# Kernel optimization log

Hardware: AMD Instinct MI355X
Metric: run time of the kernel (lower is better)

The kernel has to match this reference:

```python
import jax, jax.numpy as jnp
import numpy as np

P, H, T, B = 16, 24, 168, 4096


def _lstm(x, W_ih, W_hh, b_ih, b_hh):
    # x: [B, T, F]; PyTorch gate order i, f, g, o; returns all hidden states [B, T, H]
    Bsz = x.shape[0]
    Hd = W_hh.shape[1]
    # batch the input GEMM over all timesteps
    xg = jnp.einsum('btf,gf->btg', x, W_ih) + b_ih + b_hh  # [B, T, 4H]

    def step(carry, xt):
        h, c = carry
        g = xt + h @ W_hh.T  # [B, 4H]
        i, f, gg, o = jnp.split(g, 4, axis=-1)
        c = jax.nn.sigmoid(f) * c + jax.nn.sigmoid(i) * jnp.tanh(gg)
        h = jax.nn.sigmoid(o) * jnp.tanh(c)
        return (h, c), h

    h0 = jnp.zeros((Bsz, Hd), x.dtype)
    _, hs = jax.lax.scan(step, (h0, h0), jnp.swapaxes(xg, 0, 1))
    return jnp.swapaxes(hs, 0, 1)  # [B, T, H]


def setup_inputs() -> dict:
    key = jax.random.key(0)
    ks = jax.random.split(key, 14)
    s1 = 1.0 / np.sqrt(H)
    u = lambda k, shape: jax.random.uniform(k, shape, jnp.float32, -s1, s1)
    return {
        'x': jax.random.normal(ks[0], (B, T, P), jnp.float32),
        'W_ih1': u(ks[1], (4 * H, P)), 'W_hh1': u(ks[2], (4 * H, H)),
        'b_ih1': u(ks[3], (4 * H,)), 'b_hh1': u(ks[4], (4 * H,)),
        'W_ih2': u(ks[5], (4 * H, H)), 'W_hh2': u(ks[6], (4 * H, H)),
        'b_ih2': u(ks[7], (4 * H,)), 'b_hh2': u(ks[8], (4 * H,)),
        'W1': u(ks[9], (16, H)), 'b1': u(ks[10], (16,)),
        'W2': u(ks[11], (H, 16)), 'b2': u(ks[12], (H,)),
    }


def reference(x, W_ih1, W_hh1, b_ih1, b_hh1, W_ih2, W_hh2, b_ih2, b_hh2, W1, b1, W2, b2):
    h = jnp.tanh(_lstm(x, W_ih1, W_hh1, b_ih1, b_hh1))       # [B, T, H]
    h = jnp.tanh(_lstm(h, W_ih2, W_hh2, b_ih2, b_hh2))       # [B, T, H]
    h = h[:, -1, :]                                           # [B, H]
    h = jax.nn.relu(h @ W1.T + b1)                            # [B, 16]; dropout = identity (eval mode)
    out = h @ W2.T + b2                                       # [B, 24]
    return out.reshape(out.shape[0], -1, 1)                   # [B, 24, 1]
```

## Files before the change

### kernel.cpp

```cpp
#include <hip/hip_runtime.h>

constexpr int T = 168;
constexpr int P = 16;
constexpr int H = 24;

typedef float v2f __attribute__((ext_vector_type(2)));

__device__ __forceinline__ v2f mk2(float a, float b) { v2f r; r[0] = a; r[1] = b; return r; }
__device__ __forceinline__ v2f bc2(float a)          { v2f r; r[0] = a; r[1] = a; return r; }
__device__ __forceinline__ v2f pkfma(v2f a, v2f b, v2f c) {
    return __builtin_elementwise_fma(a, b, c);
}

__device__ __forceinline__ float rcp_f(float x) { return __builtin_amdgcn_rcpf(x); }
__device__ __forceinline__ float sigm_f(float x) { return rcp_f(1.f + __expf(-x)); }
__device__ __forceinline__ float tanh_fast(float x) {
    return fmaf(2.f, rcp_f(1.f + __expf(-2.f * x)), -1.f);
}

#define KEEP2(v) asm volatile("" : "+v"(v))
#define LDS_SYNC() asm volatile("s_waitcnt lgkmcnt(0)" ::: "memory")

#define PK4(acc_, v4_, w_, b_) do {                       \
    acc_ = pkfma(bc2((v4_).x), (w_)[(b_)],     acc_);     \
    acc_ = pkfma(bc2((v4_).y), (w_)[(b_) + 1], acc_);     \
    acc_ = pkfma(bc2((v4_).z), (w_)[(b_) + 2], acc_);     \
    acc_ = pkfma(bc2((v4_).w), (w_)[(b_) + 3], acc_); } while (0)

__device__ __forceinline__ void act_store(v2f g, int lane, int half,
                                          float& c, float* hdst, float* tdst)
{
    float a0 = sigm_f(g[0]);
    float px = (half == 0) ? g[1] + g[1] : g[1];
    float sv = sigm_f(px);
    float a1 = (half == 0) ? sv + sv - 1.f : sv;
    float fa = __shfl(a0, lane + 24);
    float oa = __shfl(a1, lane + 24);
    c = fmaf(fa, c, a0 * a1);
    float hv = oa * tanh_fast(c);
    if (tdst) {
        float th = tanh_fast(hv);
        if (lane < H) { hdst[lane] = hv; tdst[lane] = th; }
    } else {
        if (lane < H) hdst[lane] = hv;
    }
}

__global__ __attribute__((amdgpu_flat_work_group_size(128, 128),
                          amdgpu_waves_per_eu(4, 4)))
void lstm2_split2(const float* __restrict__ x,
                  const float* __restrict__ Wih1, const float* __restrict__ Whh1,
                  const float* __restrict__ bih1, const float* __restrict__ bhh1,
                  const float* __restrict__ Wih2, const float* __restrict__ Whh2,
                  const float* __restrict__ bih2, const float* __restrict__ bhh2,
                  const float* __restrict__ W1, const float* __restrict__ b1,
                  const float* __restrict__ W2, const float* __restrict__ b2,
                  float* __restrict__ out)
{
    const int tid  = threadIdx.x;
    const int wid  = tid >> 6;
    const int lane = tid & 63;
    const int s    = (lane < 48) ? lane : 47;
    const int u    = s % H;
    const int half = s / H;
    const int q0   = half * H + u;
    const int q1   = (2 + half) * H + u;
    const int rowA = blockIdx.x * 2;
    const int rowB = rowA + 1;

    const float* __restrict__ Wi = wid ? Wih2 : Wih1;
    const float* __restrict__ Wh = wid ? Whh2 : Whh1;
    const float* __restrict__ bi = wid ? bih2 : bih1;
    const float* __restrict__ bh = wid ? bhh2 : bhh1;
    const int nin = wid ? H : P;

    v2f w[48];
    #pragma unroll
    for (int k = 0; k < H; ++k)
        w[k] = (k < nin) ? mk2(Wi[q0 * nin + k], Wi[q1 * nin + k]) : bc2(0.f);
    #pragma unroll
    for (int k = 0; k < H; ++k)
        w[H + k] = mk2(Wh[q0 * H + k], Wh[q1 * H + k]);
    v2f bias = mk2(bi[q0] + bh[q0], bi[q1] + bh[q1]);

    #pragma unroll
    for (int k = 0; k < 48; ++k) KEEP2(w[k]);
    KEEP2(bias);

    __shared__ __align__(16) float h1s[2][32];
    __shared__ __align__(16) float t1s[2][2][32];
    __shared__ __align__(16) float h2s[2][32];

    const float* __restrict__ xA = x + (size_t)rowA * T * P;
    const float* __restrict__ xB = x + (size_t)rowB * T * P;

    float cA = 0.f, cB = 0.f;

    if (wid == 0) {
        v2f gA = bias, gB = bias;
        #pragma unroll
        for (int j = 0; j < P / 4; ++j) {
            float4 va = ((const float4*)xA)[j];
            float4 vb = ((const float4*)xB)[j];
            PK4(gA, va, w, 4 * j);
            PK4(gB, vb, w, 4 * j);
        }
        act_store(gA, lane, half, cA, h1s[0], t1s[0][0]);
        act_store(gB, lane, half, cB, h1s[1], t1s[0][1]);
    } else {
        if (lane < H) { h2s[0][lane] = 0.f; h2s[1][lane] = 0.f; }
    }
    LDS_SYNC();
    __builtin_amdgcn_s_barrier();

    for (int t = 1; t < T; ++t) {
        if (wid == 0) {
            v2f gA = bias, gB = bias;
            const float4* xa4 = (const float4*)(xA + t * P);
            const float4* xb4 = (const float4*)(xB + t * P);
            #pragma unroll
            for (int j = 0; j < P / 4; ++j) {
                float4 va = xa4[j];
                float4 vb = xb4[j];
                PK4(gA, va, w, 4 * j);
                PK4(gB, vb, w, 4 * j);
            }
            #pragma unroll
            for (int k = 0; k < H / 4; ++k) {
                float4 ha = ((const float4*)h1s[0])[k];
                float4 hb = ((const float4*)h1s[1])[k];
                PK4(gA, ha, w, H + 4 * k);
                PK4(gB, hb, w, H + 4 * k);
            }
            act_store(gA, lane, half, cA, h1s[0], t1s[t & 1][0]);
            act_store(gB, lane, half, cB, h1s[1], t1s[t & 1][1]);
        } else {
            v2f fA = bias, fB = bias;
            const float* t1a = t1s[(t - 1) & 1][0];
            const float* t1b = t1s[(t - 1) & 1][1];
            #pragma unroll
            for (int k = 0; k < H / 4; ++k) {
                float4 ta  = ((const float4*)t1a)[k];
                float4 tb4 = ((const float4*)t1b)[k];
                PK4(fA, ta,  w, 4 * k);
                PK4(fB, tb4, w, 4 * k);
            }
            #pragma unroll
            for (int k = 0; k < H / 4; ++k) {
                float4 ha = ((const float4*)h2s[0])[k];
                float4 hb = ((const float4*)h2s[1])[k];
                PK4(fA, ha, w, H + 4 * k);
                PK4(fB, hb, w, H + 4 * k);
            }
            act_store(fA, lane, half, cA, h2s[0], nullptr);
            act_store(fB, lane, half, cB, h2s[1], nullptr);
        }
        LDS_SYNC();
        __builtin_amdgcn_s_barrier();
    }

    if (wid == 1) {
        v2f fA = bias, fB = bias;
        const float* t1a = t1s[(T - 1) & 1][0];
        const float* t1b = t1s[(T - 1) & 1][1];
        #pragma unroll
        for (int k = 0; k < H / 4; ++k) {
            float4 ta  = ((const float4*)t1a)[k];
            float4 tb4 = ((const float4*)t1b)[k];
            PK4(fA, ta,  w, 4 * k);
            PK4(fB, tb4, w, 4 * k);
        }
        #pragma unroll
        for (int k = 0; k < H / 4; ++k) {
            float4 ha = ((const float4*)h2s[0])[k];
            float4 hb = ((const float4*)h2s[1])[k];
            PK4(fA, ha, w, H + 4 * k);
            PK4(fB, hb, w, H + 4 * k);
        }
        act_store(fA, lane, half, cA, h2s[0], nullptr);
        act_store(fB, lane, half, cB, h2s[1], nullptr);
        LDS_SYNC();

        if (lane < H) {
            t1s[0][0][lane] = tanh_fast(h2s[0][lane]);
            t1s[0][1][lane] = tanh_fast(h2s[1][lane]);
        }
        LDS_SYNC();
        if (lane < 16) {
            float accA = b1[lane], accB = b1[lane];
            #pragma unroll
            for (int j = 0; j < H; ++j) {
                float wv = W1[lane * H + j];
                accA = fmaf(t1s[0][0][j], wv, accA);
                accB = fmaf(t1s[0][1][j], wv, accB);
            }
            h1s[0][lane] = fmaxf(accA, 0.f);
            h1s[1][lane] = fmaxf(accB, 0.f);
        }
        LDS_SYNC();
        if (lane < H) {
            float accA = b2[lane], accB = b2[lane];
            #pragma unroll
            for (int j = 0; j < 16; ++j) {
                float wv = W2[lane * 16 + j];
                accA = fmaf(h1s[0][j], wv, accA);
                accB = fmaf(h1s[1][j], wv, accB);
            }
            out[(size_t)rowA * H + lane] = accA;
            out[(size_t)rowB * H + lane] = accB;
        }
    }
}

extern "C" void kernel_launch(void* const* d_in, const int* in_sizes, int n_in,
                              void* d_out, int out_size, void* d_ws, size_t ws_size,
                              hipStream_t stream)
{
    const float* x    = (const float*)d_in[0];
    const float* Wih1 = (const float*)d_in[1];
    const float* Whh1 = (const float*)d_in[2];
    const float* bih1 = (const float*)d_in[3];
    const float* bhh1 = (const float*)d_in[4];
    const float* Wih2 = (const float*)d_in[5];
    const float* Whh2 = (const float*)d_in[6];
    const float* bih2 = (const float*)d_in[7];
    const float* bhh2 = (const float*)d_in[8];
    const float* W1   = (const float*)d_in[9];
    const float* b1   = (const float*)d_in[10];
    const float* W2   = (const float*)d_in[11];
    const float* b2   = (const float*)d_in[12];
    float* out = (float*)d_out;

    const int B = in_sizes[0] / (T * P);
    hipLaunchKernelGGL(lstm2_split2, dim3(B / 2), dim3(128), 0, stream,
                       x, Wih1, Whh1, bih1, bhh1, Wih2, Whh2, bih2, bhh2,
                       W1, b1, W2, b2, out);
}
```

Measured before the change: 447.1 us.

## Process two timesteps per workgroup barrier in the layer-pipelined LSTM

```diff
diff --git a/kernel.cpp b/kernel.cpp
--- a/kernel.cpp
+++ b/kernel.cpp
@@ -46,9 +46,40 @@
     }
 }
 
+#define L1_STEP(xrow_, hrow_, c_, tdst_) do {                          \
+    v2f g_ = bias;                                                     \
+    const float4* x4_ = (const float4*)(xrow_);                        \
+    _Pragma("unroll")                                                  \
+    for (int j_ = 0; j_ < P / 4; ++j_) {                               \
+        float4 v_ = x4_[j_];                                           \
+        PK4(g_, v_, w, 4 * j_);                                        \
+    }                                                                  \
+    _Pragma("unroll")                                                  \
+    for (int k_ = 0; k_ < H / 4; ++k_) {                               \
+        float4 hv_ = ((const float4*)(hrow_))[k_];                     \
+        PK4(g_, hv_, w, H + 4 * k_);                                   \
+    }                                                                  \
+    act_store(g_, lane, half, c_, hrow_, tdst_);                       \
+} while (0)
+
+#define L2_STEP(trow_, hrow_, c_) do {                                 \
+    v2f f_ = bias;                                                     \
+    _Pragma("unroll")                                                  \
+    for (int k_ = 0; k_ < H / 4; ++k_) {                               \
+        float4 tv_ = ((const float4*)(trow_))[k_];                     \
+        PK4(f_, tv_, w, 4 * k_);                                       \
+    }                                                                  \
+    _Pragma("unroll")                                                  \
+    for (int k_ = 0; k_ < H / 4; ++k_) {                               \
+        float4 hv_ = ((const float4*)(hrow_))[k_];                     \
+        PK4(f_, hv_, w, H + 4 * k_);                                   \
+    }                                                                  \
+    act_store(f_, lane, half, c_, hrow_, nullptr);                     \
+} while (0)
+
 __global__ __attribute__((amdgpu_flat_work_group_size(128, 128),
-                          amdgpu_waves_per_eu(4, 4)))
-void lstm2_split2(const float* __restrict__ x,
+                          amdgpu_num_vgpr(128)))
+void lstm2_split4(const float* __restrict__ x,
                   const float* __restrict__ Wih1, const float* __restrict__ Whh1,
                   const float* __restrict__ bih1, const float* __restrict__ bhh1,
                   const float* __restrict__ Wih2, const float* __restrict__ Whh2,
@@ -88,7 +119,7 @@
     KEEP2(bias);
 
     __shared__ __align__(16) float h1s[2][32];
-    __shared__ __align__(16) float t1s[2][2][32];
+    __shared__ __align__(16) float t1s[2][2][2][32];
     __shared__ __align__(16) float h2s[2][32];
 
     const float* __restrict__ xA = x + (size_t)rowA * T * P;
@@ -97,93 +128,64 @@
     float cA = 0.f, cB = 0.f;
 
     if (wid == 0) {
-        v2f gA = bias, gB = bias;
-        #pragma unroll
-        for (int j = 0; j < P / 4; ++j) {
-            float4 va = ((const float4*)xA)[j];
-            float4 vb = ((const float4*)xB)[j];
-            PK4(gA, va, w, 4 * j);
-            PK4(gB, vb, w, 4 * j);
-        }
-        act_store(gA, lane, half, cA, h1s[0], t1s[0][0]);
-        act_store(gB, lane, half, cB, h1s[1], t1s[0][1]);
+        {
+            v2f g = bias;
+            #pragma unroll
+            for (int j = 0; j < P / 4; ++j) {
+                float4 v = ((const float4*)xA)[j];
+                PK4(g, v, w, 4 * j);
+            }
+            act_store(g, lane, half, cA, h1s[0], t1s[0][0][0]);
+        }
+        {
+            v2f g = bias;
+            #pragma unroll
+            for (int j = 0; j < P / 4; ++j) {
+                float4 v = ((const float4*)xB)[j];
+                PK4(g, v, w, 4 * j);
+            }
+            act_store(g, lane, half, cB, h1s[1], t1s[0][0][1]);
+        }
+        LDS_SYNC();
+        L1_STEP(xA + P, h1s[0], cA, t1s[0][1][0]);
+        L1_STEP(xB + P, h1s[1], cB, t1s[0][1][1]);
     } else {
         if (lane < H) { h2s[0][lane] = 0.f; h2s[1][lane] = 0.f; }
     }
     LDS_SYNC();
     __builtin_amdgcn_s_barrier();
 
-    for (int t = 1; t < T; ++t) {
+    for (int ss = 1; ss < T / 2; ++ss) {
         if (wid == 0) {
-            v2f gA = bias, gB = bias;
-            const float4* xa4 = (const float4*)(xA + t * P);
-            const float4* xb4 = (const float4*)(xB + t * P);
-            #pragma unroll
-            for (int j = 0; j < P / 4; ++j) {
-                float4 va = xa4[j];
-                float4 vb = xb4[j];
-                PK4(gA, va, w, 4 * j);
-                PK4(gB, vb, w, 4 * j);
-            }
-            #pragma unroll
-            for (int k = 0; k < H / 4; ++k) {
-                float4 ha = ((const float4*)h1s[0])[k];
-                float4 hb = ((const float4*)h1s[1])[k];
-                PK4(gA, ha, w, H + 4 * k);
-                PK4(gB, hb, w, H + 4 * k);
-            }
-            act_store(gA, lane, half, cA, h1s[0], t1s[t & 1][0]);
-            act_store(gB, lane, half, cB, h1s[1], t1s[t & 1][1]);
+            const int ta = 2 * ss;
+            L1_STEP(xA + ta * P,       h1s[0], cA, t1s[ss & 1][0][0]);
+            L1_STEP(xB + ta * P,       h1s[1], cB, t1s[ss & 1][0][1]);
+            LDS_SYNC();
+            L1_STEP(xA + (ta + 1) * P, h1s[0], cA, t1s[ss & 1][1][0]);
+            L1_STEP(xB + (ta + 1) * P, h1s[1], cB, t1s[ss & 1][1][1]);
         } else {
-            v2f fA = bias, fB = bias;
-            const float* t1a = t1s[(t - 1) & 1][0];
-            const float* t1b = t1s[(t - 1) & 1][1];
-            #pragma unroll
-            for (int k = 0; k < H / 4; ++k) {
-                float4 ta  = ((const float4*)t1a)[k];
-                float4 tb4 = ((const float4*)t1b)[k];
-                PK4(fA, ta,  w, 4 * k);
-                PK4(fB, tb4, w, 4 * k);
-            }
-            #pragma unroll
-            for (int k = 0; k < H / 4; ++k) {
-                float4 ha = ((const float4*)h2s[0])[k];
-                float4 hb = ((const float4*)h2s[1])[k];
-                PK4(fA, ha, w, H + 4 * k);
-                PK4(fB, hb, w, H + 4 * k);
-            }
-            act_store(fA, lane, half, cA, h2s[0], nullptr);
-            act_store(fB, lane, half, cB, h2s[1], nullptr);
+            const int pb = (ss - 1) & 1;
+            L2_STEP(t1s[pb][0][0], h2s[0], cA);
+            L2_STEP(t1s[pb][0][1], h2s[1], cB);
+            LDS_SYNC();
+            L2_STEP(t1s[pb][1][0], h2s[0], cA);
+            L2_STEP(t1s[pb][1][1], h2s[1], cB);
         }
         LDS_SYNC();
         __builtin_amdgcn_s_barrier();
     }
 
     if (wid == 1) {
-        v2f fA = bias, fB = bias;
-        const float* t1a = t1s[(T - 1) & 1][0];
-        const float* t1b = t1s[(T - 1) & 1][1];
-        #pragma unroll
-        for (int k = 0; k < H / 4; ++k) {
-            float4 ta  = ((const float4*)t1a)[k];
-            float4 tb4 = ((const float4*)t1b)[k];
-            PK4(fA, ta,  w, 4 * k);
-            PK4(fB, tb4, w, 4 * k);
-        }
-        #pragma unroll
-        for (int k = 0; k < H / 4; ++k) {
-            float4 ha = ((const float4*)h2s[0])[k];
-            float4 hb = ((const float4*)h2s[1])[k];
-            PK4(fA, ha, w, H + 4 * k);
-            PK4(fB, hb, w, H + 4 * k);
-        }
-        act_store(fA, lane, half, cA, h2s[0], nullptr);
-        act_store(fB, lane, half, cB, h2s[1], nullptr);
+        L2_STEP(t1s[1][0][0], h2s[0], cA);
+        L2_STEP(t1s[1][0][1], h2s[1], cB);
+        LDS_SYNC();
+        L2_STEP(t1s[1][1][0], h2s[0], cA);
+        L2_STEP(t1s[1][1][1], h2s[1], cB);
         LDS_SYNC();
 
         if (lane < H) {
-            t1s[0][0][lane] = tanh_fast(h2s[0][lane]);
-            t1s[0][1][lane] = tanh_fast(h2s[1][lane]);
+            t1s[0][0][0][lane] = tanh_fast(h2s[0][lane]);
+            t1s[0][0][1][lane] = tanh_fast(h2s[1][lane]);
         }
         LDS_SYNC();
         if (lane < 16) {
@@ -191,8 +193,8 @@
             #pragma unroll
             for (int j = 0; j < H; ++j) {
                 float wv = W1[lane * H + j];
-                accA = fmaf(t1s[0][0][j], wv, accA);
-                accB = fmaf(t1s[0][1][j], wv, accB);
+                accA = fmaf(t1s[0][0][0][j], wv, accA);
+                accB = fmaf(t1s[0][0][1][j], wv, accB);
             }
             h1s[0][lane] = fmaxf(accA, 0.f);
             h1s[1][lane] = fmaxf(accB, 0.f);
@@ -232,7 +234,7 @@
     float* out = (float*)d_out;
 
     const int B = in_sizes[0] / (T * P);
-    hipLaunchKernelGGL(lstm2_split2, dim3(B / 2), dim3(128), 0, stream,
+    hipLaunchKernelGGL(lstm2_split4, dim3(B / 2), dim3(128), 0, stream,
                        x, Wih1, Whh1, bih1, bhh1, Wih2, Whh2, bih2, bhh2,
                        W1, b1, W2, b2, out);
 }
```

Result: faster. 360.2 us (-19.4%).
